# Performance work log

Measured on AMD Instinct MI355X. Metric: run time of the kernel, lower is better.

Reference implementation:

```python
import jax, jax.numpy as jnp
import numpy as np

B, C, H, W = 4, 16, 32, 32
I = 256    # input_embedding_dim
E = 256    # decoded_embed_dim
L = 4      # num_blocks
S = 4      # scaling_factor
NCH = 64   # num_channels (embedding rows)
HID = 4 * E


def setup_inputs() -> dict:
    key = jax.random.key(0)
    ks = jax.random.split(key, 10)
    f = lambda k, sh: jax.random.normal(k, sh, jnp.float32) * 0.02
    return dict(
        x=jax.random.normal(ks[0], (B, I, H, W), jnp.float32),
        indices=jax.random.randint(ks[1], (B, C), 0, NCH),
        hk_w=f(ks[2], (NCH, I * E)),          # Hyperkernel weight embedding table
        hk_b=f(ks[3], (NCH, E)),              # Hyperkernel bias embedding table
        dw_w=f(ks[4], (L, E, 1, 7, 7)),       # depthwise conv weights per block
        dw_b=jnp.zeros((L, E), jnp.float32),
        ln_g=jnp.ones((L, E), jnp.float32),
        ln_b=jnp.zeros((L, E), jnp.float32),
        fc1_w=f(ks[5], (L, HID, E)),
        fc1_b=jnp.zeros((L, HID), jnp.float32),
        grn_g=jnp.zeros((L, HID), jnp.float32),  # GRN gamma init zeros (as in torch)
        grn_b=jnp.zeros((L, HID), jnp.float32),
        fc2_w=f(ks[6], (L, E, HID)),
        fc2_b=jnp.zeros((L, E), jnp.float32),
        pred_w=f(ks[7], (S * S * 2, E)),      # 1x1 conv == linear over channels
        pred_b=jnp.zeros((S * S * 2,), jnp.float32),
    )


def _grn(x, g, b, eps=1e-6):
    # x: [N,H,W,D]; L2 norm over spatial dims per channel
    gx = jnp.sqrt(jnp.sum(x * x, axis=(1, 2), keepdims=True))  # [N,1,1,D]
    nx = gx / (jnp.mean(gx, axis=-1, keepdims=True) + eps)
    return g * (x * nx) + b + x


def _convnext_block(x, dw_w, dw_b, ln_g, ln_b, fc1_w, fc1_b, grn_g, grn_b, fc2_w, fc2_b):
    # x: [N,E,H,W]
    res = x
    x = jax.lax.conv_general_dilated(
        x, dw_w, window_strides=(1, 1), padding=[(3, 3), (3, 3)],
        dimension_numbers=('NCHW', 'OIHW', 'NCHW'), feature_group_count=E)
    x = x + dw_b[None, :, None, None]
    x = x.transpose(0, 2, 3, 1)  # NHWC
    mu = x.mean(-1, keepdims=True)
    var = jnp.mean((x - mu) ** 2, axis=-1, keepdims=True)
    x = (x - mu) / jnp.sqrt(var + 1e-5) * ln_g + ln_b
    x = jax.nn.gelu(x @ fc1_w.T + fc1_b, approximate=False)
    x = _grn(x, grn_g, grn_b)
    x = x @ fc2_w.T + fc2_b
    return x.transpose(0, 3, 1, 2) + res


def reference(x, indices, hk_w, hk_b, dw_w, dw_b, ln_g, ln_b, fc1_w, fc1_b,
              grn_g, grn_b, fc2_w, fc2_b, pred_w, pred_b):
    # Hyperkernel, decoder/linear path: gather per-channel weights, einsum route
    w = hk_w[indices].reshape(B, C, I, E)                       # [B,C,I,E]
    h = jnp.einsum('bihw,bcie->bcehw', x, w)                    # [B,C,E,H,W]
    h = h + hk_b[indices][..., None, None]
    h = h.reshape(B * C, E, H, W)
    for l in range(L):
        h = _convnext_block(h, dw_w[l], dw_b[l], ln_g[l], ln_b[l],
                            fc1_w[l], fc1_b[l], grn_g[l], grn_b[l],
                            fc2_w[l], fc2_b[l])
    # pred 1x1 conv -> pixel-shuffle style rearrange
    p = jnp.einsum('nehw,oe->nohw', h, pred_w) + pred_b[None, :, None, None]
    p = p.reshape(B, C, S, S, 2, H, W)
    p = p.transpose(0, 1, 5, 2, 6, 3, 4)  # bcxyohw -> bchxwyo
    return p.reshape(B, C, H * S, W * S, 2)
```

## Files before the change

### kernel.cpp

```cpp
#include <hip/hip_runtime.h>
#include <hip/hip_bf16.h>
#include <math.h>


typedef __attribute__((ext_vector_type(8))) __bf16 bf16x8;
typedef __attribute__((ext_vector_type(4))) float f32x4;

__device__ __forceinline__ short f2bf(float f) {
  unsigned u = __float_as_uint(f);
  unsigned r = (u + 0x7FFFu + ((u >> 16) & 1u)) >> 16;
  return (short)r;
}
__device__ __forceinline__ float bf2f(short s) {
  return __uint_as_float(((unsigned)(unsigned short)s) << 16);
}
__device__ __forceinline__ int pack2(short a, short b) {
  return (int)(unsigned short)a | ((int)(unsigned short)b << 16);
}
__device__ __forceinline__ float gelu(float x) {
  float t = __builtin_fmaf(0.0713548162f * x * x, x, 1.59576912f * x);
  return x / (1.f + __expf(-t));
}

__device__ __forceinline__ void gload16(const short* g, short* l) {
  __builtin_amdgcn_global_load_lds(
      (const __attribute__((address_space(1))) void*)(g),
      (__attribute__((address_space(3))) void*)(l), 16, 0, 0);
}

__device__ __forceinline__ float block_sum(float v, float* red) {
#pragma unroll
  for (int o = 32; o > 0; o >>= 1) v += __shfl_down(v, o);
  int lane = threadIdx.x & 63, w = threadIdx.x >> 6;
  int nw = blockDim.x >> 6;
  if (lane == 0) red[w] = v;
  __syncthreads();
  if (threadIdx.x == 0) {
    float s = 0.f;
    for (int i = 0; i < nw; ++i) s += red[i];
    red[0] = s;
  }
  __syncthreads();
  float s = red[0];
  __syncthreads();
  return s;
}

template <int K>
__device__ __forceinline__ void gemm_core(const short* __restrict__ A, const short* __restrict__ Bt,
                                          int m0, int n0, short* As, short* Bs, f32x4 acc[4][4]) {
  const int tid = threadIdx.x;
  const int lane = tid & 63, wave = tid >> 6;
  const int wr = wave >> 1, wc = wave & 1;
  const int lr = lane & 15, kg = lane >> 4;
#pragma unroll
  for (int mi = 0; mi < 4; ++mi)
#pragma unroll
    for (int ni = 0; ni < 4; ++ni) acc[mi][ni] = f32x4{0.f, 0.f, 0.f, 0.f};
  const int sr = lane >> 2, sc = (lane & 3) * 8;
  const int ra0 = wave * 16, ra1 = wave * 16 + 64;
  const short* Ab = A + (size_t)m0 * K;
  const short* Bb = Bt + (size_t)n0 * K;
  for (int k0 = 0; k0 < K; k0 += 32) {
    gload16(Ab + (size_t)(ra0 + sr) * K + k0 + sc, As + ra0 * 32);
    gload16(Ab + (size_t)(ra1 + sr) * K + k0 + sc, As + ra1 * 32);
    gload16(Bb + (size_t)(ra0 + sr) * K + k0 + sc, Bs + ra0 * 32);
    gload16(Bb + (size_t)(ra1 + sr) * K + k0 + sc, Bs + ra1 * 32);
    __syncthreads();
    bf16x8 af[4], bfr[4];
#pragma unroll
    for (int mi = 0; mi < 4; ++mi) af[mi] = *(const bf16x8*)&As[(wr * 64 + mi * 16 + lr) * 32 + kg * 8];
#pragma unroll
    for (int ni = 0; ni < 4; ++ni) bfr[ni] = *(const bf16x8*)&Bs[(wc * 64 + ni * 16 + lr) * 32 + kg * 8];
#pragma unroll
    for (int mi = 0; mi < 4; ++mi)
#pragma unroll
      for (int ni = 0; ni < 4; ++ni)
        acc[mi][ni] = __builtin_amdgcn_mfma_f32_16x16x32_bf16(af[mi], bfr[ni], acc[mi][ni], 0, 0, 0);
    __syncthreads();
  }
}

template <int K>
__device__ __forceinline__ void gemm_core_n64(const short* __restrict__ A, const short* __restrict__ Bt,
                                              int m0, int n0, short* As, short* Bs, f32x4 acc[4][2]) {
  const int tid = threadIdx.x;
  const int lane = tid & 63, wave = tid >> 6;
  const int wr = wave >> 1, wc = wave & 1;
  const int lr = lane & 15, kg = lane >> 4;
#pragma unroll
  for (int mi = 0; mi < 4; ++mi)
#pragma unroll
    for (int ni = 0; ni < 2; ++ni) acc[mi][ni] = f32x4{0.f, 0.f, 0.f, 0.f};
  const int sr = lane >> 2, sc = (lane & 3) * 8;
  const int ra0 = wave * 16, ra1 = wave * 16 + 64;
  const short* Ab = A + (size_t)m0 * K;
  const short* Bb = Bt + (size_t)n0 * K;
  for (int k0 = 0; k0 < K; k0 += 32) {
    gload16(Ab + (size_t)(ra0 + sr) * K + k0 + sc, As + ra0 * 32);
    gload16(Ab + (size_t)(ra1 + sr) * K + k0 + sc, As + ra1 * 32);
    gload16(Bb + (size_t)(ra0 + sr) * K + k0 + sc, Bs + ra0 * 32);
    __syncthreads();
    bf16x8 af[4], bfr[2];
#pragma unroll
    for (int mi = 0; mi < 4; ++mi) af[mi] = *(const bf16x8*)&As[(wr * 64 + mi * 16 + lr) * 32 + kg * 8];
#pragma unroll
    for (int ni = 0; ni < 2; ++ni) bfr[ni] = *(const bf16x8*)&Bs[(wc * 32 + ni * 16 + lr) * 32 + kg * 8];
#pragma unroll
    for (int mi = 0; mi < 4; ++mi)
#pragma unroll
      for (int ni = 0; ni < 2; ++ni)
        acc[mi][ni] = __builtin_amdgcn_mfma_f32_16x16x32_bf16(af[mi], bfr[ni], acc[mi][ni], 0, 0, 0);
    __syncthreads();
  }
}

__global__ void k_cvt_w(const float* __restrict__ fc1w, const float* __restrict__ fc2w,
                        short* __restrict__ w1b, short* __restrict__ w2b) {
  int i = blockIdx.x * 256 + threadIdx.x;
  w1b[i] = f2bf(fc1w[i]);
  w2b[i] = f2bf(fc2w[i]);
}

__global__ void k_prep_xt(const float* __restrict__ x, short* __restrict__ xTb) {
  __shared__ float tile[32][33];
  int tx = threadIdx.x & 31, ty = threadIdx.x >> 5;
  int p0 = blockIdx.x * 32, i0 = blockIdx.y * 32, b = blockIdx.z;
#pragma unroll
  for (int r = 0; r < 4; ++r) {
    int i = ty + r * 8;
    tile[i][tx] = x[((size_t)b * 256 + i0 + i) * 1024 + p0 + tx];
  }
  __syncthreads();
#pragma unroll
  for (int r = 0; r < 4; ++r) {
    int p = ty + r * 8;
    xTb[((size_t)b * 1024 + p0 + p) * 256 + i0 + tx] = f2bf(tile[tx][p]);
  }
}

__global__ void k_prep_wt(const float* __restrict__ hkw, const int* __restrict__ idx,
                          short* __restrict__ Wt) {
  __shared__ float tile[32][33];
  int tx = threadIdx.x & 31, ty = threadIdx.x >> 5;
  int e0 = blockIdx.x * 32, i0 = blockIdx.y * 32, n = blockIdx.z;
  int ch = idx[n];
#pragma unroll
  for (int r = 0; r < 4; ++r) {
    int i = ty + r * 8;
    tile[i][tx] = hkw[(size_t)ch * 65536 + (size_t)(i0 + i) * 256 + e0 + tx];
  }
  __syncthreads();
#pragma unroll
  for (int r = 0; r < 4; ++r) {
    int e = ty + r * 8;
    Wt[((size_t)n * 256 + e0 + e) * 256 + i0 + tx] = f2bf(tile[tx][e]);
  }
}

__global__ void k_prep_misc(const float* __restrict__ grng, const float* __restrict__ grnb,
                            const float* __restrict__ fc2w, int* __restrict__ flag,
                            float* __restrict__ cvec) {
  __shared__ float red[8];
  int l = blockIdx.y;
  if (blockIdx.x == 0) {
    float any = 0.f;
    for (int d = threadIdx.x; d < 1024; d += 256)
      any += (grng[l * 1024 + d] != 0.f) ? 1.f : 0.f;
    float tot = block_sum(any, red);
    if (threadIdx.x == 0) flag[l] = (tot > 0.f) ? 1 : 0;
  } else {
    int e = blockIdx.x - 1;
    float s = 0.f;
    for (int d = threadIdx.x; d < 1024; d += 256)
      s += fc2w[((size_t)(l * 256 + e) << 10) + d] * grnb[l * 1024 + d];
    float tot = block_sum(s, red);
    if (threadIdx.x == 0) cvec[l * 256 + e] = tot;
  }
}

__global__ void __launch_bounds__(256) k_hypm(const short* __restrict__ Wt, const short* __restrict__ xTb,
                                              const int* __restrict__ idx, const float* __restrict__ hkb,
                                              short* __restrict__ hb) {
  __shared__ short As[4096], Bs[4096];
  f32x4 acc[4][4];
  int n = blockIdx.z;
  int m0 = blockIdx.y * 128, n0 = blockIdx.x * 128;
  gemm_core<256>(Wt + (size_t)n * 65536, xTb + (size_t)(n >> 4) * 262144, m0, n0, As, Bs, acc);
  int ch = idx[n];
  const int lane = threadIdx.x & 63, wave = threadIdx.x >> 6;
  const int wr = wave >> 1, wc = wave & 1, lr = lane & 15, kg = lane >> 4;
#pragma unroll
  for (int mi = 0; mi < 4; ++mi) {
    int ebase = m0 + wr * 64 + mi * 16 + kg * 4;
#pragma unroll
    for (int ni = 0; ni < 4; ++ni) {
      int p = n0 + wc * 64 + ni * 16 + lr;
      f32x4 v = acc[mi][ni];
#pragma unroll
      for (int r = 0; r < 4; ++r)
        hb[((size_t)(n * 256 + ebase + r) << 10) + p] = f2bf(v[r] + hkb[ch * 256 + ebase + r]);
    }
  }
}

__global__ void __launch_bounds__(256) k_conv(const short* __restrict__ hb, const float* __restrict__ dww,
                                              const float* __restrict__ dwb, short* __restrict__ tc, int l) {
  __shared__ float sm[38][40];
  int e = blockIdx.x, n = blockIdx.y;
  const short* plane = hb + (((size_t)(n * 256 + e)) << 10);
  const float* wv = dww + ((size_t)(l * 256 + e)) * 49;
  float w[49];
#pragma unroll
  for (int i = 0; i < 49; ++i) w[i] = wv[i];
  int tid = threadIdx.x;
  for (int i = tid; i < 38 * 40; i += 256) ((float*)sm)[i] = 0.f;
  __syncthreads();
  for (int i = tid; i < 1024; i += 256) sm[(i >> 5) + 3][(i & 31) + 3] = bf2f(plane[i]);
  __syncthreads();
  int x = tid & 31, y0 = (tid >> 5) * 4;
  float bias = dwb[l * 256 + e];
  float acc0 = bias, acc1 = bias, acc2 = bias, acc3 = bias;
#pragma unroll
  for (int r = 0; r < 10; ++r) {
#pragma unroll
    for (int c = 0; c < 7; ++c) {
      float v = sm[y0 + r][x + c];
      if (r <= 6)           acc0 += v * w[r * 7 + c];
      if (r >= 1 && r <= 7) acc1 += v * w[(r - 1) * 7 + c];
      if (r >= 2 && r <= 8) acc2 += v * w[(r - 2) * 7 + c];
      if (r >= 3)           acc3 += v * w[(r - 3) * 7 + c];
    }
  }
  short* outp = tc + (((size_t)(n * 256 + e)) << 10) + y0 * 32 + x;
  outp[0]  = f2bf(acc0);
  outp[32] = f2bf(acc1);
  outp[64] = f2bf(acc2);
  outp[96] = f2bf(acc3);
}

__global__ void __launch_bounds__(256) k_ln(const short* __restrict__ tc, const float* __restrict__ lng,
                                            const float* __restrict__ lnb, short* __restrict__ tb,
                                            float* __restrict__ gx, const int* __restrict__ flag, int l) {
  __shared__ float smT[32][261];
  __shared__ float muS[32], rsS[32];
  int n = blockIdx.y, p0 = blockIdx.x * 32;
  int tid = threadIdx.x;
  if (blockIdx.x == 0 && flag[l] != 0) {
#pragma unroll
    for (int r = 0; r < 4; ++r) gx[n * 1024 + r * 256 + tid] = 0.f;
  }
  const short* base = tc + ((size_t)n << 18) + p0;
  for (int i = tid; i < 8192; i += 256) {
    int e = i >> 5, p = i & 31;
    smT[p][e] = bf2f(base[(e << 10) + p]);
  }
  __syncthreads();
  {
    int j = tid & 7, p = tid >> 3;
    float s = 0.f, q = 0.f;
#pragma unroll
    for (int i = 0; i < 32; ++i) {
      float v = smT[p][j + i * 8];
      s += v; q += v * v;
    }
    s += __shfl_xor(s, 1); q += __shfl_xor(q, 1);
    s += __shfl_xor(s, 2); q += __shfl_xor(q, 2);
    s += __shfl_xor(s, 4); q += __shfl_xor(q, 4);
    if (j == 0) {
      float mu = s * (1.f / 256.f);
      float var = q * (1.f / 256.f) - mu * mu;
      muS[p] = mu;
      rsS[p] = rsqrtf(fmaxf(var, 0.f) + 1e-5f);
    }
  }
  __syncthreads();
  for (int i = tid; i < 8192; i += 256) {
    int p = i >> 8, e = i & 255;
    float v = (smT[p][e] - muS[p]) * rsS[p] * lng[l * 256 + e] + lnb[l * 256 + e];
    tb[((size_t)(n * 1024 + p0 + p)) * 256 + e] = f2bf(v);
  }
}

__global__ void __launch_bounds__(256) k_gx1(const short* __restrict__ w1b, const short* __restrict__ tb,
                                             const float* __restrict__ fc1b, float* __restrict__ gx,
                                             const int* __restrict__ flag, int l) {
  if (flag[l] == 0) return;
  __shared__ short As[4096], Bs[4096];
  f32x4 acc[4][4];
  int m0 = blockIdx.y * 128, n0 = blockIdx.x * 128;
  gemm_core<256>(w1b + (size_t)l * 262144, tb, m0, n0, As, Bs, acc);
  const int lane = threadIdx.x & 63, wave = threadIdx.x >> 6;
  const int wr = wave >> 1, kg = lane >> 4;
  int n = (n0 >> 10);
#pragma unroll
  for (int mi = 0; mi < 4; ++mi) {
    int dbase = m0 + wr * 64 + mi * 16 + kg * 4;
#pragma unroll
    for (int ni = 0; ni < 4; ++ni) {
      f32x4 v = acc[mi][ni];
#pragma unroll
      for (int r = 0; r < 4; ++r) {
        float g = gelu(v[r] + fc1b[l * 1024 + dbase + r]);
        atomicAdd(&gx[n * 1024 + dbase + r], g * g);
      }
    }
  }
}

__global__ void k_nx(const float* __restrict__ gx, float* __restrict__ nx,
                     const int* __restrict__ flag, int l) {
  int n = blockIdx.x, tid = threadIdx.x;
  if (flag[l] == 0) {
    for (int d = tid; d < 1024; d += 256) nx[n * 1024 + d] = 0.f;
    return;
  }
  __shared__ float red[8];
  __shared__ float sv[1024];
  float s = 0.f;
  for (int d = tid; d < 1024; d += 256) {
    float v = sqrtf(gx[n * 1024 + d]);
    sv[d] = v; s += v;
  }
  float tot = block_sum(s, red);
  float mean = tot * (1.f / 1024.f);
  for (int d = tid; d < 1024; d += 256) nx[n * 1024 + d] = sv[d] / (mean + 1e-6f);
}

__global__ void __launch_bounds__(256) k_fc1(const short* __restrict__ w1b, const short* __restrict__ tb,
                                             const float* __restrict__ fc1b, const float* __restrict__ grng,
                                             const float* __restrict__ nx, short* __restrict__ u,
                                             int l, int cbase) {
  __shared__ short As[4096], Bs[4096];
  f32x4 acc[4][4];
  int m0 = blockIdx.y * 128, n0 = blockIdx.x * 128;
  gemm_core<256>(w1b + (size_t)l * 262144, tb + (size_t)cbase * 256, m0, n0, As, Bs, acc);
  const int lane = threadIdx.x & 63, wave = threadIdx.x >> 6;
  const int wr = wave >> 1, wc = wave & 1, lr = lane & 15, kg = lane >> 4;
  int nimg = (cbase + n0) >> 10;
#pragma unroll
  for (int mi = 0; mi < 4; ++mi) {
    int dbase = m0 + wr * 64 + mi * 16 + kg * 4;
    float b0 = fc1b[l * 1024 + dbase + 0], b1 = fc1b[l * 1024 + dbase + 1];
    float b2 = fc1b[l * 1024 + dbase + 2], b3 = fc1b[l * 1024 + dbase + 3];
    float a0 = 1.f + grng[l * 1024 + dbase + 0] * nx[nimg * 1024 + dbase + 0];
    float a1 = 1.f + grng[l * 1024 + dbase + 1] * nx[nimg * 1024 + dbase + 1];
    float a2 = 1.f + grng[l * 1024 + dbase + 2] * nx[nimg * 1024 + dbase + 2];
    float a3 = 1.f + grng[l * 1024 + dbase + 3] * nx[nimg * 1024 + dbase + 3];
#pragma unroll
    for (int ni = 0; ni < 4; ++ni) {
      int pl = n0 + wc * 64 + ni * 16 + lr;
      f32x4 v = acc[mi][ni];
      short4 sv;
      sv.x = f2bf(gelu(v[0] + b0) * a0);
      sv.y = f2bf(gelu(v[1] + b1) * a1);
      sv.z = f2bf(gelu(v[2] + b2) * a2);
      sv.w = f2bf(gelu(v[3] + b3) * a3);
      *(short4*)&u[(size_t)pl * 1024 + dbase] = sv;
    }
  }
}

template <int LAST>
__global__ void __launch_bounds__(256) k_fc2(const short* __restrict__ w2b, const short* __restrict__ u,
                                             const float* __restrict__ fc2b, const float* __restrict__ cvec,
                                             short* __restrict__ hb, short* __restrict__ ht,
                                             int l, int cbase) {
  __shared__ short As[4096], Bs[2048];
  f32x4 acc[4][2];
  int m0 = blockIdx.y * 128, n0 = blockIdx.x * 64;
  gemm_core_n64<1024>(w2b + (size_t)l * 262144, u, m0, n0, As, Bs, acc);
  const int lane = threadIdx.x & 63, wave = threadIdx.x >> 6;
  const int wr = wave >> 1, wc = wave & 1, lr = lane & 15, kg = lane >> 4;
#pragma unroll
  for (int mi = 0; mi < 4; ++mi) {
    int ebase = m0 + wr * 64 + mi * 16 + kg * 4;
    float add0 = fc2b[l * 256 + ebase + 0] + cvec[l * 256 + ebase + 0];
    float add1 = fc2b[l * 256 + ebase + 1] + cvec[l * 256 + ebase + 1];
    float add2 = fc2b[l * 256 + ebase + 2] + cvec[l * 256 + ebase + 2];
    float add3 = fc2b[l * 256 + ebase + 3] + cvec[l * 256 + ebase + 3];
#pragma unroll
    for (int ni = 0; ni < 2; ++ni) {
      int P = cbase + n0 + wc * 32 + ni * 16 + lr;
      int n = P >> 10, p = P & 1023;
      f32x4 v = acc[mi][ni];
      short* hp0 = &hb[((size_t)(n * 256 + ebase) << 10) + p];
      float r0 = v[0] + add0 + bf2f(hp0[0]);
      float r1 = v[1] + add1 + bf2f(hp0[1 << 10]);
      float r2 = v[2] + add2 + bf2f(hp0[2 << 10]);
      float r3 = v[3] + add3 + bf2f(hp0[3 << 10]);
      if (LAST) {
        short* hr = &ht[(size_t)P * 256 + ebase];
        hr[0] = f2bf(r0); hr[1] = f2bf(r1); hr[2] = f2bf(r2); hr[3] = f2bf(r3);
      } else {
        hp0[0] = f2bf(r0); hp0[1 << 10] = f2bf(r1); hp0[2 << 10] = f2bf(r2); hp0[3 << 10] = f2bf(r3);
      }
    }
  }
}

__global__ void __launch_bounds__(128) k_pred2(const short* __restrict__ ht, const float* __restrict__ pw,
                                               const float* __restrict__ pb, float* __restrict__ out) {
  __shared__ short Aw[32 * 264];
  __shared__ short Bl[256 * 32];
  int tid = threadIdx.x;
  int n0 = blockIdx.x * 256;
  for (int i = tid; i < 8192; i += 128) {
    int o = i >> 8, e = i & 255;
    Aw[o * 264 + e] = f2bf(pw[i]);
  }
  const int lane = tid & 63, wave = tid >> 6;
  const int lr = lane & 15, kg = lane >> 4;
  const int sr = lane >> 2, sc = (lane & 3) * 8;
  f32x4 acc[2][8];
#pragma unroll
  for (int mi = 0; mi < 2; ++mi)
#pragma unroll
    for (int ni = 0; ni < 8; ++ni) acc[mi][ni] = f32x4{0.f, 0.f, 0.f, 0.f};
  __syncthreads();
  for (int k0 = 0; k0 < 256; k0 += 32) {
#pragma unroll
    for (int j = 0; j < 8; ++j) {
      int rb = wave * 128 + j * 16;
      gload16(ht + (size_t)(n0 + rb + sr) * 256 + k0 + sc, Bl + rb * 32);
    }
    __syncthreads();
    bf16x8 af[2], bfr[8];
#pragma unroll
    for (int mi = 0; mi < 2; ++mi) af[mi] = *(const bf16x8*)&Aw[(mi * 16 + lr) * 264 + k0 + kg * 8];
#pragma unroll
    for (int ni = 0; ni < 8; ++ni) bfr[ni] = *(const bf16x8*)&Bl[(wave * 128 + ni * 16 + lr) * 32 + kg * 8];
#pragma unroll
    for (int mi = 0; mi < 2; ++mi)
#pragma unroll
      for (int ni = 0; ni < 8; ++ni)
        acc[mi][ni] = __builtin_amdgcn_mfma_f32_16x16x32_bf16(af[mi], bfr[ni], acc[mi][ni], 0, 0, 0);
    __syncthreads();
  }
#pragma unroll
  for (int mi = 0; mi < 2; ++mi) {
#pragma unroll
    for (int ni = 0; ni < 8; ++ni) {
      int P = n0 + wave * 128 + ni * 16 + lr;
      int n = P >> 10, p = P & 1023;
      int y = p >> 5, xx = p & 31;
      f32x4 v = acc[mi][ni];
#pragma unroll
      for (int r = 0; r < 4; ++r) {
        int o = mi * 16 + kg * 4 + r;
        int s1 = o >> 3, s2 = (o >> 1) & 3, tt = o & 1;
        size_t oi = (((size_t)n * 128 + y * 4 + s1) * 128 + xx * 4 + s2) * 2 + tt;
        out[oi] = v[r] + pb[o];
      }
    }
  }
}

extern "C" void kernel_launch(void* const* d_in, const int* in_sizes, int n_in,
                              void* d_out, int out_size, void* d_ws, size_t ws_size,
                              hipStream_t stream) {
  const float* x    = (const float*)d_in[0];
  const int*   idx  = (const int*)d_in[1];
  const float* hkw  = (const float*)d_in[2];
  const float* hkb  = (const float*)d_in[3];
  const float* dww  = (const float*)d_in[4];
  const float* dwb  = (const float*)d_in[5];
  const float* lng  = (const float*)d_in[6];
  const float* lnb  = (const float*)d_in[7];
  const float* fc1w = (const float*)d_in[8];
  const float* fc1b = (const float*)d_in[9];
  const float* grng = (const float*)d_in[10];
  const float* grnb = (const float*)d_in[11];
  const float* fc2w = (const float*)d_in[12];
  const float* fc2b = (const float*)d_in[13];
  const float* pw   = (const float*)d_in[14];
  const float* pb   = (const float*)d_in[15];
  float* out = (float*)d_out;

  char* ws = (char*)d_ws;
  short* hb   = (short*)(ws);
  short* tb   = (short*)(ws + (32ull << 20));
  short* u    = (short*)(ws + (64ull << 20));
  short* tc   = (short*)(ws + (64ull << 20));
  short* Wt   = (short*)(ws + (64ull << 20));
  short* xTb  = (short*)(ws + (72ull << 20));
  short* w1b  = (short*)(ws + (128ull << 20));
  short* w2b  = (short*)(ws + (130ull << 20));
  float* gx   = (float*)(ws + (132ull << 20));
  float* nx   = (float*)(ws + (132ull << 20) + (1 << 18));
  float* cvec = (float*)(ws + (132ull << 20) + (2 << 18));
  int*   flag = (int*)  (ws + (132ull << 20) + (2 << 18) + 4096);

  k_cvt_w<<<4096, 256, 0, stream>>>(fc1w, fc2w, w1b, w2b);
  k_prep_misc<<<dim3(257, 4), 256, 0, stream>>>(grng, grnb, fc2w, flag, cvec);
  k_prep_xt<<<dim3(32, 8, 4), 256, 0, stream>>>(x, xTb);
  k_prep_wt<<<dim3(8, 8, 64), 256, 0, stream>>>(hkw, idx, Wt);
  k_hypm<<<dim3(8, 2, 64), 256, 0, stream>>>(Wt, xTb, idx, hkb, hb);
  for (int l = 0; l < 4; ++l) {
    k_conv<<<dim3(256, 64), 256, 0, stream>>>(hb, dww, dwb, tc, l);
    k_ln<<<dim3(32, 64), 256, 0, stream>>>(tc, lng, lnb, tb, gx, flag, l);
    k_gx1<<<dim3(512, 8), 256, 0, stream>>>(w1b, tb, fc1b, gx, flag, l);
    k_nx<<<64, 256, 0, stream>>>(gx, nx, flag, l);
    for (int c = 0; c < 2; ++c) {
      int cbase = c * 32768;
      k_fc1<<<dim3(256, 8), 256, 0, stream>>>(w1b, tb, fc1b, grng, nx, u, l, cbase);
      if (l < 3)
        k_fc2<0><<<dim3(512, 2), 256, 0, stream>>>(w2b, u, fc2b, cvec, hb, tb, l, cbase);
      else
        k_fc2<1><<<dim3(512, 2), 256, 0, stream>>>(w2b, u, fc2b, cvec, hb, tb, l, cbase);
    }
  }
  k_pred2<<<256, 128, 0, stream>>>(tb, pw, pb, out);
}
```

Before: 936.1 us.

## Remap GEMM blocks per XCD, stage fc1 output in LDS, vectorize conv plane load

fc1 and fc2 launches become 1D grids whose block index is remapped so that consecutive N tiles sharing the same M tiles are placed on the same XCD. The intent is better L2 reuse of the weight and activation tiles. The fc1 epilogue now writes GELU/GRN results into an LDS tile and then stores full coalesced 128-element rows of u, replacing scattered 8-byte stores. The trade-off is an extra LDS buffer and two barriers per block. The depthwise conv also loads its plane as 32-bit pairs instead of single 16-bit values.

```diff
diff --git a/kernel.cpp b/kernel.cpp
--- a/kernel.cpp
+++ b/kernel.cpp
@@ -216,7 +216,16 @@
   int tid = threadIdx.x;
   for (int i = tid; i < 38 * 40; i += 256) ((float*)sm)[i] = 0.f;
   __syncthreads();
-  for (int i = tid; i < 1024; i += 256) sm[(i >> 5) + 3][(i & 31) + 3] = bf2f(plane[i]);
+  {
+    const int* plane32 = (const int*)plane;
+    for (int i = tid; i < 512; i += 256) {
+      int v = plane32[i];
+      int p = i * 2;
+      int iy = p >> 5, ix = p & 31;
+      sm[iy + 3][ix + 3] = bf2f((short)(v & 0xffff));
+      sm[iy + 3][ix + 4] = bf2f((short)(v >> 16));
+    }
+  }
   __syncthreads();
   int x = tid & 31, y0 = (tid >> 5) * 4;
   float bias = dwb[l * 256 + e];
@@ -332,31 +341,53 @@
                                              const float* __restrict__ nx, short* __restrict__ u,
                                              int l, int cbase) {
   __shared__ short As[4096], Bs[4096];
+  __shared__ short Ue[64 * 136];
   f32x4 acc[4][4];
-  int m0 = blockIdx.y * 128, n0 = blockIdx.x * 128;
+  int bid = blockIdx.x;
+  int xcd = bid & 7, loc = bid >> 3;
+  int nt = (xcd << 5) + (loc >> 3);
+  int mt = loc & 7;
+  int m0 = mt * 128, n0 = nt * 128;
   gemm_core<256>(w1b + (size_t)l * 262144, tb + (size_t)cbase * 256, m0, n0, As, Bs, acc);
-  const int lane = threadIdx.x & 63, wave = threadIdx.x >> 6;
+  const int tid = threadIdx.x;
+  const int lane = tid & 63, wave = tid >> 6;
   const int wr = wave >> 1, wc = wave & 1, lr = lane & 15, kg = lane >> 4;
   int nimg = (cbase + n0) >> 10;
 #pragma unroll
-  for (int mi = 0; mi < 4; ++mi) {
-    int dbase = m0 + wr * 64 + mi * 16 + kg * 4;
-    float b0 = fc1b[l * 1024 + dbase + 0], b1 = fc1b[l * 1024 + dbase + 1];
-    float b2 = fc1b[l * 1024 + dbase + 2], b3 = fc1b[l * 1024 + dbase + 3];
-    float a0 = 1.f + grng[l * 1024 + dbase + 0] * nx[nimg * 1024 + dbase + 0];
-    float a1 = 1.f + grng[l * 1024 + dbase + 1] * nx[nimg * 1024 + dbase + 1];
-    float a2 = 1.f + grng[l * 1024 + dbase + 2] * nx[nimg * 1024 + dbase + 2];
-    float a3 = 1.f + grng[l * 1024 + dbase + 3] * nx[nimg * 1024 + dbase + 3];
-#pragma unroll
-    for (int ni = 0; ni < 4; ++ni) {
-      int pl = n0 + wc * 64 + ni * 16 + lr;
-      f32x4 v = acc[mi][ni];
-      short4 sv;
-      sv.x = f2bf(gelu(v[0] + b0) * a0);
-      sv.y = f2bf(gelu(v[1] + b1) * a1);
-      sv.z = f2bf(gelu(v[2] + b2) * a2);
-      sv.w = f2bf(gelu(v[3] + b3) * a3);
-      *(short4*)&u[(size_t)pl * 1024 + dbase] = sv;
+  for (int half = 0; half < 2; ++half) {
+    if (half) __syncthreads();
+    if (wc == half) {
+#pragma unroll
+      for (int mi = 0; mi < 4; ++mi) {
+        int dbase = m0 + wr * 64 + mi * 16 + kg * 4;
+        float b0 = fc1b[l * 1024 + dbase + 0], b1 = fc1b[l * 1024 + dbase + 1];
+        float b2 = fc1b[l * 1024 + dbase + 2], b3 = fc1b[l * 1024 + dbase + 3];
+        float a0 = 1.f + grng[l * 1024 + dbase + 0] * nx[nimg * 1024 + dbase + 0];
+        float a1 = 1.f + grng[l * 1024 + dbase + 1] * nx[nimg * 1024 + dbase + 1];
+        float a2 = 1.f + grng[l * 1024 + dbase + 2] * nx[nimg * 1024 + dbase + 2];
+        float a3 = 1.f + grng[l * 1024 + dbase + 3] * nx[nimg * 1024 + dbase + 3];
+        int dloc = wr * 64 + mi * 16 + kg * 4;
+#pragma unroll
+        for (int ni = 0; ni < 4; ++ni) {
+          int pxl = ni * 16 + lr;
+          f32x4 v = acc[mi][ni];
+          short4 sv;
+          sv.x = f2bf(gelu(v[0] + b0) * a0);
+          sv.y = f2bf(gelu(v[1] + b1) * a1);
+          sv.z = f2bf(gelu(v[2] + b2) * a2);
+          sv.w = f2bf(gelu(v[3] + b3) * a3);
+          *(short4*)&Ue[pxl * 136 + dloc] = sv;
+        }
+      }
+    }
+    __syncthreads();
+#pragma unroll
+    for (int it = 0; it < 8; ++it) {
+      int idx = it * 256 + tid;
+      int px = idx >> 5;
+      int dd = (idx & 31) * 4;
+      int pl = n0 + half * 64 + px;
+      *(short4*)&u[(size_t)pl * 1024 + m0 + dd] = *(const short4*)&Ue[px * 136 + dd];
     }
   }
 }
@@ -368,7 +399,11 @@
                                              int l, int cbase) {
   __shared__ short As[4096], Bs[2048];
   f32x4 acc[4][2];
-  int m0 = blockIdx.y * 128, n0 = blockIdx.x * 64;
+  int bid = blockIdx.x;
+  int xcd = bid & 7, loc = bid >> 3;
+  int nt = (xcd << 6) + (loc >> 1);
+  int mt = loc & 1;
+  int m0 = mt * 128, n0 = nt * 64;
   gemm_core_n64<1024>(w2b + (size_t)l * 262144, u, m0, n0, As, Bs, acc);
   const int lane = threadIdx.x & 63, wave = threadIdx.x >> 6;
   const int wr = wave >> 1, wc = wave & 1, lr = lane & 15, kg = lane >> 4;
@@ -503,11 +538,11 @@
     k_nx<<<64, 256, 0, stream>>>(gx, nx, flag, l);
     for (int c = 0; c < 2; ++c) {
       int cbase = c * 32768;
-      k_fc1<<<dim3(256, 8), 256, 0, stream>>>(w1b, tb, fc1b, grng, nx, u, l, cbase);
+      k_fc1<<<2048, 256, 0, stream>>>(w1b, tb, fc1b, grng, nx, u, l, cbase);
       if (l < 3)
-        k_fc2<0><<<dim3(512, 2), 256, 0, stream>>>(w2b, u, fc2b, cvec, hb, tb, l, cbase);
+        k_fc2<0><<<1024, 256, 0, stream>>>(w2b, u, fc2b, cvec, hb, tb, l, cbase);
       else
-        k_fc2<1><<<dim3(512, 2), 256, 0, stream>>>(w2b, u, fc2b, cvec, hb, tb, l, cbase);
+        k_fc2<1><<<1024, 256, 0, stream>>>(w2b, u, fc2b, cvec, hb, tb, l, cbase);
     }
   }
   k_pred2<<<256, 128, 0, stream>>>(tb, pw, pb, out);
```

New measurement: 989.8 us. 5.7% more time.
